# Kernel tuning notes

Hardware: AMD Instinct MI355X
Metric: run time of the kernel (lower is better)

The kernel has to match this reference:

```python
import jax, jax.numpy as jnp
import numpy as np

N = 50000   # nodes
D = 256     # embed_dim
H = 256     # hidden_dim
E = 250000  # edges per relation type
T = 3       # edge types
NEG_SLOPE = 0.2  # PyG GATConv default


def setup_inputs() -> dict:
    key = jax.random.key(0)
    ks = jax.random.split(key, 12)
    s = lambda k, shape: jax.random.normal(k, shape, jnp.float32) * 0.05
    z = jax.random.normal(ks[0], (N, D), jnp.float32)
    ei = jax.random.randint(ks[1], (T, 2, E), 0, N, dtype=jnp.int32)
    W1 = s(ks[2], (T, D, H)); as1 = s(ks[3], (T, H)); ad1 = s(ks[4], (T, H))
    b1 = jnp.zeros((T, H), jnp.float32)
    W2 = s(ks[5], (T, H, H)); as2 = s(ks[6], (T, H)); ad2 = s(ks[7], (T, H))
    b2 = jnp.zeros((T, H), jnp.float32)
    Wh = s(ks[8], (H, 1)); bh = jnp.zeros((1,), jnp.float32)
    return dict(z=z, ei=ei, W1=W1, as1=as1, ad1=ad1, b1=b1,
                W2=W2, as2=as2, ad2=ad2, b2=b2, Wh=Wh, bh=bh)


def gat_conv(x, ei, W, a_s, a_d, b):
    # PyG GATConv, heads=1, no self loops: h = x W; e_ij = leaky_relu(a_s.h_j + a_d.h_i)
    # alpha = softmax over incoming edges of node i; out_i = sum_j alpha_ij h_j + bias
    src, dst = ei[0], ei[1]
    n = x.shape[0]
    h = x @ W                              # [N, H]
    a_src = h @ a_s                        # [N]
    a_dst = h @ a_d                        # [N]
    e = jax.nn.leaky_relu(a_src[src] + a_dst[dst], NEG_SLOPE)   # [E]
    m = jax.ops.segment_max(e, dst, num_segments=n)             # per-dst max
    ex = jnp.exp(e - m[dst])
    den = jax.ops.segment_sum(ex, dst, num_segments=n)
    alpha = ex / den[dst]                                       # [E]
    out = jax.ops.segment_sum(h[src] * alpha[:, None], dst, num_segments=n)
    return out + b


def layer(x, ei, W, a_s, a_d, b):
    # sum of per-type GATConv outputs, then ReLU (matches module)
    outs = jax.vmap(lambda e_, W_, s_, d_, b_: gat_conv(x, e_, W_, s_, d_, b_))(ei, W, a_s, a_d, b)
    return jax.nn.relu(outs.sum(0))


def reference(z, ei, W1, as1, ad1, b1, W2, as2, ad2, b2, Wh, bh):
    h1 = layer(z, ei, W1, as1, ad1, b1)
    h2 = layer(h1, ei, W2, as2, ad2, b2)
    return jax.nn.sigmoid(h2 @ Wh + bh).squeeze(-1)   # [N]
```

## Files before the change

### kernel.cpp

```cpp
#include <hip/hip_runtime.h>

#define GAT_N 50000
#define GAT_D 256
#define GAT_T 3
#define GAT_E 250000
#define GAT_B (GAT_T*GAT_N)
#define GAT_TOTE (GAT_T*GAT_E)
#define GAT_COLS (GAT_T*GAT_D)
#define GAT_SLOPE 0.2f

typedef unsigned short u16;
typedef unsigned int u32;
typedef __attribute__((ext_vector_type(8))) short s16x8;
typedef __attribute__((ext_vector_type(8))) __bf16 bf16x8;
typedef __attribute__((ext_vector_type(4))) float f32x4;
typedef __attribute__((ext_vector_type(2))) u32 u32x2;

__device__ __forceinline__ u16 f2bf(float f) {
    u32 x = __builtin_bit_cast(u32, f);
    u32 r = (x + 0x7fffu + ((x >> 16) & 1u)) >> 16;
    return (u16)r;
}
__device__ __forceinline__ float lo16(u32 w) {
    return __builtin_bit_cast(float, w << 16);
}
__device__ __forceinline__ float hi16(u32 w) {
    return __builtin_bit_cast(float, w & 0xffff0000u);
}

template<int CTRL>
__device__ __forceinline__ float dppadd(float x) {
    int y = __builtin_amdgcn_update_dpp(0, __builtin_bit_cast(int, x),
                                        CTRL, 0xf, 0xf, true);
    return x + __builtin_bit_cast(float, y);
}
__device__ __forceinline__ float sum16(float x) {
    x = dppadd<0xB1>(x);
    x = dppadd<0x4E>(x);
    x = dppadd<0x141>(x);
    x = dppadd<0x140>(x);
    return x;
}

__global__ void gat_prep(const float* __restrict__ W1, const float* __restrict__ W2,
                         const float* __restrict__ z, const float* __restrict__ b1,
                         const float* __restrict__ b2, u16* __restrict__ WT1b,
                         u16* __restrict__ WT2b, u16* __restrict__ zb,
                         float* __restrict__ bias3)
{
    int idx = blockIdx.x * 256 + threadIdx.x;
    if (idx < GAT_T * GAT_D * GAT_D) {
        int t = idx >> 16, r = idx & 65535;
        int h = r >> 8, d = r & 255;
        WT1b[idx] = f2bf(W1[t * 65536 + d * 256 + h]);
        WT2b[idx] = f2bf(W2[t * 65536 + d * 256 + h]);
    }
    if (idx < 2 * GAT_D) {
        const float* bb = (idx < GAT_D) ? b1 : b2;
        int c = idx & 255;
        bias3[idx] = bb[c] + bb[GAT_D + c] + bb[2 * GAT_D + c];
    }
    if (idx < GAT_N * GAT_D / 4) {
        f32x4 v = ((const f32x4*)z)[idx];
        ushort4 pk;
        pk.x = f2bf(v.x); pk.y = f2bf(v.y); pk.z = f2bf(v.z); pk.w = f2bf(v.w);
        ((ushort4*)zb)[idx] = pk;
    }
}

__global__ void gat_scatter(const int* __restrict__ ei, u32* __restrict__ deg,
                            int* __restrict__ psrc2)
{
    int idx = blockIdx.x * 256 + threadIdx.x;
    if (idx >= GAT_TOTE) return;
    int t = idx / GAT_E;
    int e = idx - t * GAT_E;
    int src = ei[t * 2 * GAT_E + e];
    int dst = ei[t * 2 * GAT_E + GAT_E + e];
    u32 slot = atomicAdd(&deg[dst], 1u);
    if (slot < 64u)
        psrc2[(size_t)dst * 64 + slot] = t * GAT_N + src;
}

__global__ __launch_bounds__(512, 4) void gat_gemm(
    const u16* __restrict__ A, const u16* __restrict__ WTb,
    u16* __restrict__ H, const float* __restrict__ as_in,
    const float* __restrict__ ad_in, float* __restrict__ part_src,
    float* __restrict__ part_dst)
{
    int lin = blockIdx.x;
    int g   = lin / 48;
    int rem = lin - g * 48;
    int bc  = rem >> 3;
    int br  = (g << 3) + (rem & 7);
    if (br >= 391) return;

    __shared__ u16 Als[2][128 * 64];
    __shared__ u16 Bls[2][128 * 64];
    int tid  = threadIdx.x;
    int wave = tid >> 6, lane = tid & 63;
    int quad = lane >> 4, l16 = lane & 15;
    int wm = wave & 1, wn = wave >> 1;
    int lrow = lane >> 3;
    int swz  = ((lane & 7) ^ lrow) * 8;

    size_t arow0 = (size_t)br * 128;
    size_t brow0 = (size_t)bc * 128;

    auto STAGE = [&](int buf, int ks) {
        int k0 = ks * 64;
        #pragma unroll
        for (int r = 0; r < 2; ++r) {
            int srow = wave * 16 + r * 8 + lrow;
            const u16* gA = A   + (arow0 + srow) * GAT_D + k0 + swz;
            const u16* gB = WTb + (brow0 + srow) * GAT_D + k0 + swz;
            u16* lA = &Als[buf][wave * 1024 + r * 512];
            u16* lB = &Bls[buf][wave * 1024 + r * 512];
#if defined(__has_builtin) && __has_builtin(__builtin_amdgcn_global_load_lds)
            __builtin_amdgcn_global_load_lds(
                (const __attribute__((address_space(1))) void*)gA,
                (__attribute__((address_space(3))) void*)lA, 16, 0, 0);
            __builtin_amdgcn_global_load_lds(
                (const __attribute__((address_space(1))) void*)gB,
                (__attribute__((address_space(3))) void*)lB, 16, 0, 0);
#else
            *(s16x8*)(lA + lane * 8) = *(const s16x8*)gA;
            *(s16x8*)(lB + lane * 8) = *(const s16x8*)gB;
#endif
        }
    };

    f32x4 acc[4][2] = {};

    STAGE(0, 0);
    #pragma unroll
    for (int ks = 0; ks < 4; ++ks) {
        int cur = ks & 1;
        if (ks < 3) {
            STAGE(cur ^ 1, ks + 1);
            asm volatile("s_waitcnt vmcnt(4)" ::: "memory");
        } else {
            asm volatile("s_waitcnt vmcnt(0)" ::: "memory");
        }
        __builtin_amdgcn_s_barrier();

        #pragma unroll
        for (int kk = 0; kk < 2; ++kk) {
            int csw8 = ((kk * 4 + quad) ^ (l16 & 7)) * 8;
            bf16x8 af[4], bf[2];
            #pragma unroll
            for (int i = 0; i < 4; ++i)
                af[i] = __builtin_bit_cast(bf16x8,
                    *(const s16x8*)(&Als[cur][(wm * 64 + i * 16 + l16) * 64 + csw8]));
            #pragma unroll
            for (int j = 0; j < 2; ++j)
                bf[j] = __builtin_bit_cast(bf16x8,
                    *(const s16x8*)(&Bls[cur][(wn * 32 + j * 16 + l16) * 64 + csw8]));
            #pragma unroll
            for (int i = 0; i < 4; ++i)
                #pragma unroll
                for (int j = 0; j < 2; ++j)
                    acc[i][j] = __builtin_amdgcn_mfma_f32_16x16x32_bf16(
                        af[i], bf[j], acc[i][j], 0, 0, 0);
        }
        if (ks < 3)
            __builtin_amdgcn_s_barrier();
    }

    int gcol0 = bc * 128 + wn * 32;
    int t   = gcol0 >> 8;
    int ch0 = gcol0 & 255;
    int c32 = bc * 4 + wn;
    u16* Ht = H + (size_t)t * GAT_N * GAT_D;
    int rowb = br * 128 + wm * 64 + quad * 4;
    #pragma unroll
    for (int i = 0; i < 4; ++i) {
        #pragma unroll
        for (int j = 0; j < 2; ++j) {
            int ch = ch0 + j * 16 + l16;
            #pragma unroll
            for (int r = 0; r < 4; ++r) {
                int row = rowb + i * 16 + r;
                if (row < GAT_N) Ht[(size_t)row * GAT_D + ch] = f2bf(acc[i][j][r]);
            }
        }
    }

    float asv[2], adv[2];
    #pragma unroll
    for (int j = 0; j < 2; ++j) {
        int ch = ch0 + j * 16 + l16;
        asv[j] = as_in[t * GAT_D + ch];
        adv[j] = ad_in[t * GAT_D + ch];
    }
    #pragma unroll
    for (int i = 0; i < 4; ++i) {
        float ps[4] = {}, pd[4] = {};
        #pragma unroll
        for (int j = 0; j < 2; ++j) {
            f32x4 a = acc[i][j];
            #pragma unroll
            for (int r = 0; r < 4; ++r) {
                ps[r] += a[r] * asv[j];
                pd[r] += a[r] * adv[j];
            }
        }
        #pragma unroll
        for (int r = 0; r < 4; ++r) {
            ps[r] = sum16(ps[r]);
            pd[r] = sum16(pd[r]);
        }
        if (l16 == 0) {
            int row = rowb + i * 16;
            #pragma unroll
            for (int r = 0; r < 4; ++r) {
                if (row + r < GAT_N) {
                    part_src[(size_t)c32 * GAT_N + row + r] = ps[r];
                    part_dst[(size_t)c32 * GAT_N + row + r] = pd[r];
                }
            }
        }
    }
}

__global__ void gat_sum(const float* __restrict__ part_src,
                        const float* __restrict__ part_dst,
                        float* __restrict__ a_src, float* __restrict__ a_dst)
{
    int idx = blockIdx.x * 256 + threadIdx.x;
    if (idx >= GAT_B) return;
    int t = idx / GAT_N;
    int n = idx - t * GAT_N;
    const float* ps = part_src + (size_t)8 * t * GAT_N;
    const float* pd = part_dst + (size_t)8 * t * GAT_N;
    float s = 0.f, d = 0.f;
    #pragma unroll
    for (int c = 0; c < 8; ++c) {
        s += ps[(size_t)c * GAT_N + n];
        d += pd[(size_t)c * GAT_N + n];
    }
    a_src[idx] = s;
    a_dst[idx] = d;
}

__global__ __launch_bounds__(64) void gat_gather(
    const u32* __restrict__ deg, const int* __restrict__ psrc2,
    const float* __restrict__ a_src, const float* __restrict__ a_dst,
    const u16* __restrict__ Hfb, const float* __restrict__ bias3,
    const float* __restrict__ Wh, const float* __restrict__ bh,
    int layer, u16* __restrict__ x2b, float* __restrict__ out)
{
    int n = blockIdx.x;
    int lane = threadIdx.x;

    u32 dv = deg[n];
    int dtot = (dv > 64u) ? 64 : (int)dv;

    int  j     = lane;
    bool valid = j < dtot;
    int  rs    = valid ? psrc2[(size_t)n * 64 + j] : 0;
    int  tj    = (rs >= GAT_N) + (rs >= 2 * GAT_N);

    float as   = a_src[rs];
    float adn  = a_dst[tj * GAT_N + n];

    const u16* Hl = Hfb + lane * 4;
    u32x2 w[8];
    #pragma unroll
    for (int u = 0; u < 8; ++u) {
        int rv = __builtin_amdgcn_readlane(rs, u);
        w[u] = *(const u32x2*)(Hl + (size_t)rv * GAT_D);
    }

    float e = as + adn;
    e = (e > 0.f) ? e : GAT_SLOPE * e;
    float ex = valid ? __expf(e) : 0.f;

    float s0 = (tj == 0) ? ex : 0.f;
    float s1 = (tj == 1) ? ex : 0.f;
    float s2 = (tj == 2) ? ex : 0.f;
    s0 = sum16(s0); s1 = sum16(s1); s2 = sum16(s2);
    #pragma unroll
    for (int d = 16; d < 64; d <<= 1) {
        s0 += __shfl_xor(s0, d);
        s1 += __shfl_xor(s1, d);
        s2 += __shfl_xor(s2, d);
    }
    float den = (tj == 0) ? s0 : ((tj == 1) ? s1 : s2);
    float alv = valid ? ex / den : 0.f;
    int av = __builtin_bit_cast(int, alv);

    float r[4] = {};
    int dpad = (dtot + 7) & ~7;
    for (int k0 = 0; ; k0 += 8) {
        float al[8]; u32x2 wc[8];
        #pragma unroll
        for (int u = 0; u < 8; ++u) {
            wc[u] = w[u];
            al[u] = __builtin_bit_cast(float,
                        __builtin_amdgcn_readlane(av, k0 + u));
        }
        bool more = (k0 + 8 < dpad);
        if (more) {
            #pragma unroll
            for (int u = 0; u < 8; ++u) {
                int rv = __builtin_amdgcn_readlane(rs, k0 + 8 + u);
                w[u] = *(const u32x2*)(Hl + (size_t)rv * GAT_D);
            }
        }
        #pragma unroll
        for (int u = 0; u < 8; ++u) {
            r[0] += al[u] * lo16(wc[u].x);
            r[1] += al[u] * hi16(wc[u].x);
            r[2] += al[u] * lo16(wc[u].y);
            r[3] += al[u] * hi16(wc[u].y);
        }
        if (!more) break;
    }

    int c0 = lane * 4;
    const float* b3 = bias3 + layer * GAT_D;
    float v[4];
    #pragma unroll
    for (int i = 0; i < 4; ++i) v[i] = fmaxf(r[i] + b3[c0 + i], 0.f);

    if (layer == 0) {
        u16 pk[4];
        #pragma unroll
        for (int i = 0; i < 4; ++i) pk[i] = f2bf(v[i]);
        *(ushort4*)(x2b + (size_t)n * GAT_D + c0) = *(ushort4*)pk;
    } else {
        float wsum = 0.f;
        #pragma unroll
        for (int i = 0; i < 4; ++i) wsum += v[i] * Wh[c0 + i];
        wsum = sum16(wsum);
        wsum += __shfl_xor(wsum, 16);
        wsum += __shfl_xor(wsum, 32);
        if (lane == 0) out[n] = 1.0f / (1.0f + __expf(-(wsum + bh[0])));
    }
}

__global__ void PyGTypeSpecificGAT_80075370266775_kernel() {}

extern "C" void kernel_launch(void* const* d_in, const int* in_sizes, int n_in,
                              void* d_out, int out_size, void* d_ws, size_t ws_size,
                              hipStream_t stream)
{
    (void)in_sizes; (void)n_in; (void)out_size; (void)ws_size;
    const float* z   = (const float*)d_in[0];
    const int*   ei  = (const int*)d_in[1];
    const float* W1  = (const float*)d_in[2];
    const float* as1 = (const float*)d_in[3];
    const float* ad1 = (const float*)d_in[4];
    const float* b1  = (const float*)d_in[5];
    const float* W2  = (const float*)d_in[6];
    const float* as2 = (const float*)d_in[7];
    const float* ad2 = (const float*)d_in[8];
    const float* b2  = (const float*)d_in[9];
    const float* Wh  = (const float*)d_in[10];
    const float* bh  = (const float*)d_in[11];
    float* out = (float*)d_out;

    char* p = (char*)d_ws;
    u16*  Hfb  = (u16*)p;  p += (size_t)GAT_T * GAT_N * GAT_D * 2;
    u16*  x2b  = (u16*)p;  p += (size_t)GAT_N * GAT_D * 2;
    u16*  zb   = (u16*)p;  p += (size_t)GAT_N * GAT_D * 2;
    float* part_src = (float*)p; p += (size_t)24 * GAT_N * 4;
    float* part_dst = (float*)p; p += (size_t)24 * GAT_N * 4;
    float* a_src = (float*)p; p += (size_t)GAT_B * 4;
    float* a_dst = (float*)p; p += (size_t)GAT_B * 4;
    u32*  deg  = (u32*)p;  p += (size_t)GAT_N * 4;
    int*  psrc2 = (int*)p; p += (size_t)GAT_N * 64 * 4;
    u16*  WT1b = (u16*)p;  p += (size_t)GAT_COLS * GAT_D * 2;
    u16*  WT2b = (u16*)p;  p += (size_t)GAT_COLS * GAT_D * 2;
    float* bias3 = (float*)p; p += 2 * GAT_D * 4;

    const int EDGE_BLKS = (GAT_TOTE + 255) / 256;
    const int BUCK_BLKS = (GAT_B + 255) / 256;
    const int PREP_BLKS = (GAT_N * GAT_D / 4 + 255) / 256;

    hipMemsetAsync(deg, 0, (size_t)GAT_N * 4, stream);
    gat_prep<<<PREP_BLKS, 256, 0, stream>>>(W1, W2, z, b1, b2, WT1b, WT2b,
                                            zb, bias3);
    gat_scatter<<<EDGE_BLKS, 256, 0, stream>>>(ei, deg, psrc2);

    const int GEMM_BLKS = 49 * 48;

    for (int layer = 0; layer < 2; ++layer) {
        const u16*   A   = (layer == 0) ? zb   : x2b;
        const u16*   WTb = (layer == 0) ? WT1b : WT2b;
        const float* as_ = (layer == 0) ? as1  : as2;
        const float* ad_ = (layer == 0) ? ad1  : ad2;

        gat_gemm<<<GEMM_BLKS, 512, 0, stream>>>(A, WTb, Hfb, as_, ad_,
                                                part_src, part_dst);
        gat_sum<<<BUCK_BLKS, 256, 0, stream>>>(part_src, part_dst,
                                               a_src, a_dst);
        gat_gather<<<GAT_N, 64, 0, stream>>>(deg, psrc2,
                                             a_src, a_dst, Hfb, bias3,
                                             Wh, bh, layer, x2b, out);
    }
}
```

Before: 362.1 us.

## Fuse edge scatter into prep and replace partial-sum kernel with atomics

The edge bucketing (degree count and source slot fill) moves into the prep kernel, which removes one launch. The GEMM epilogue now atomically adds its per-column-block attention partials straight into zeroed a_src/a_dst arrays, so the separate gat_sum kernel and its partial buffers go away. Per-layer attention buffers are zeroed by one combined memset. This trades two launches and a pass over the partial buffers for float atomic contention and a non-deterministic summation order.

```diff
diff --git a/kernel.cpp b/kernel.cpp
--- a/kernel.cpp
+++ b/kernel.cpp
@@ -44,9 +44,10 @@
 
 __global__ void gat_prep(const float* __restrict__ W1, const float* __restrict__ W2,
                          const float* __restrict__ z, const float* __restrict__ b1,
-                         const float* __restrict__ b2, u16* __restrict__ WT1b,
-                         u16* __restrict__ WT2b, u16* __restrict__ zb,
-                         float* __restrict__ bias3)
+                         const float* __restrict__ b2, const int* __restrict__ ei,
+                         u16* __restrict__ WT1b, u16* __restrict__ WT2b,
+                         u16* __restrict__ zb, u32* __restrict__ deg,
+                         int* __restrict__ psrc2, float* __restrict__ bias3)
 {
     int idx = blockIdx.x * 256 + threadIdx.x;
     if (idx < GAT_T * GAT_D * GAT_D) {
@@ -60,6 +61,15 @@
         int c = idx & 255;
         bias3[idx] = bb[c] + bb[GAT_D + c] + bb[2 * GAT_D + c];
     }
+    if (idx < GAT_TOTE) {
+        int t = idx / GAT_E;
+        int e = idx - t * GAT_E;
+        int src = ei[t * 2 * GAT_E + e];
+        int dst = ei[t * 2 * GAT_E + GAT_E + e];
+        u32 slot = atomicAdd(&deg[dst], 1u);
+        if (slot < 64u)
+            psrc2[(size_t)dst * 64 + slot] = t * GAT_N + src;
+    }
     if (idx < GAT_N * GAT_D / 4) {
         f32x4 v = ((const f32x4*)z)[idx];
         ushort4 pk;
@@ -68,25 +78,11 @@
     }
 }
 
-__global__ void gat_scatter(const int* __restrict__ ei, u32* __restrict__ deg,
-                            int* __restrict__ psrc2)
-{
-    int idx = blockIdx.x * 256 + threadIdx.x;
-    if (idx >= GAT_TOTE) return;
-    int t = idx / GAT_E;
-    int e = idx - t * GAT_E;
-    int src = ei[t * 2 * GAT_E + e];
-    int dst = ei[t * 2 * GAT_E + GAT_E + e];
-    u32 slot = atomicAdd(&deg[dst], 1u);
-    if (slot < 64u)
-        psrc2[(size_t)dst * 64 + slot] = t * GAT_N + src;
-}
-
 __global__ __launch_bounds__(512, 4) void gat_gemm(
     const u16* __restrict__ A, const u16* __restrict__ WTb,
     u16* __restrict__ H, const float* __restrict__ as_in,
-    const float* __restrict__ ad_in, float* __restrict__ part_src,
-    float* __restrict__ part_dst)
+    const float* __restrict__ ad_in, float* __restrict__ a_s,
+    float* __restrict__ a_d)
 {
     int lin = blockIdx.x;
     int g   = lin / 48;
@@ -170,7 +166,6 @@
     int gcol0 = bc * 128 + wn * 32;
     int t   = gcol0 >> 8;
     int ch0 = gcol0 & 255;
-    int c32 = bc * 4 + wn;
     u16* Ht = H + (size_t)t * GAT_N * GAT_D;
     int rowb = br * 128 + wm * 64 + quad * 4;
     #pragma unroll
@@ -215,32 +210,12 @@
             #pragma unroll
             for (int r = 0; r < 4; ++r) {
                 if (row + r < GAT_N) {
-                    part_src[(size_t)c32 * GAT_N + row + r] = ps[r];
-                    part_dst[(size_t)c32 * GAT_N + row + r] = pd[r];
+                    atomicAdd(&a_s[t * GAT_N + row + r], ps[r]);
+                    atomicAdd(&a_d[t * GAT_N + row + r], pd[r]);
                 }
             }
         }
     }
-}
-
-__global__ void gat_sum(const float* __restrict__ part_src,
-                        const float* __restrict__ part_dst,
-                        float* __restrict__ a_src, float* __restrict__ a_dst)
-{
-    int idx = blockIdx.x * 256 + threadIdx.x;
-    if (idx >= GAT_B) return;
-    int t = idx / GAT_N;
-    int n = idx - t * GAT_N;
-    const float* ps = part_src + (size_t)8 * t * GAT_N;
-    const float* pd = part_dst + (size_t)8 * t * GAT_N;
-    float s = 0.f, d = 0.f;
-    #pragma unroll
-    for (int c = 0; c < 8; ++c) {
-        s += ps[(size_t)c * GAT_N + n];
-        d += pd[(size_t)c * GAT_N + n];
-    }
-    a_src[idx] = s;
-    a_dst[idx] = d;
 }
 
 __global__ __launch_bounds__(64) void gat_gather(
@@ -365,24 +340,24 @@
     u16*  Hfb  = (u16*)p;  p += (size_t)GAT_T * GAT_N * GAT_D * 2;
     u16*  x2b  = (u16*)p;  p += (size_t)GAT_N * GAT_D * 2;
     u16*  zb   = (u16*)p;  p += (size_t)GAT_N * GAT_D * 2;
-    float* part_src = (float*)p; p += (size_t)24 * GAT_N * 4;
-    float* part_dst = (float*)p; p += (size_t)24 * GAT_N * 4;
-    float* a_src = (float*)p; p += (size_t)GAT_B * 4;
-    float* a_dst = (float*)p; p += (size_t)GAT_B * 4;
+    char* zero_base = p;
     u32*  deg  = (u32*)p;  p += (size_t)GAT_N * 4;
+    float* a0s = (float*)p; p += (size_t)GAT_B * 4;
+    float* a0d = (float*)p; p += (size_t)GAT_B * 4;
+    float* a1s = (float*)p; p += (size_t)GAT_B * 4;
+    float* a1d = (float*)p; p += (size_t)GAT_B * 4;
+    size_t zbytes = (size_t)(p - zero_base);
     int*  psrc2 = (int*)p; p += (size_t)GAT_N * 64 * 4;
     u16*  WT1b = (u16*)p;  p += (size_t)GAT_COLS * GAT_D * 2;
     u16*  WT2b = (u16*)p;  p += (size_t)GAT_COLS * GAT_D * 2;
     float* bias3 = (float*)p; p += 2 * GAT_D * 4;
 
-    const int EDGE_BLKS = (GAT_TOTE + 255) / 256;
-    const int BUCK_BLKS = (GAT_B + 255) / 256;
     const int PREP_BLKS = (GAT_N * GAT_D / 4 + 255) / 256;
 
-    hipMemsetAsync(deg, 0, (size_t)GAT_N * 4, stream);
-    gat_prep<<<PREP_BLKS, 256, 0, stream>>>(W1, W2, z, b1, b2, WT1b, WT2b,
-                                            zb, bias3);
-    gat_scatter<<<EDGE_BLKS, 256, 0, stream>>>(ei, deg, psrc2);
+    hipMemsetAsync(zero_base, 0, zbytes, stream);
+    gat_prep<<<PREP_BLKS, 256, 0, stream>>>(W1, W2, z, b1, b2, ei,
+                                            WT1b, WT2b, zb, deg, psrc2,
+                                            bias3);
 
     const int GEMM_BLKS = 49 * 48;
 
@@ -391,13 +366,13 @@
         const u16*   WTb = (layer == 0) ? WT1b : WT2b;
         const float* as_ = (layer == 0) ? as1  : as2;
         const float* ad_ = (layer == 0) ? ad1  : ad2;
+        float* aS = (layer == 0) ? a0s : a1s;
+        float* aD = (layer == 0) ? a0d : a1d;
 
         gat_gemm<<<GEMM_BLKS, 512, 0, stream>>>(A, WTb, Hfb, as_, ad_,
-                                                part_src, part_dst);
-        gat_sum<<<BUCK_BLKS, 256, 0, stream>>>(part_src, part_dst,
-                                               a_src, a_dst);
-        gat_gather<<<GAT_N, 64, 0, stream>>>(deg, psrc2,
-                                             a_src, a_dst, Hfb, bias3,
-                                             Wh, bh, layer, x2b, out);
-    }
-}
+                                                aS, aD);
+        gat_gather<<<GAT_N, 64, 0, stream>>>(deg, psrc2, aS, aD,
+                                             Hfb, bias3, Wh, bh,
+                                             layer, x2b, out);
+    }
+}
```

After: 381.4 us. 5.3% more time.
